# Kernel optimization log

Hardware: AMD Instinct MI355X
Metric: run time of the kernel (lower is better)

The kernel has to match this reference:

```python
import jax, jax.numpy as jnp
import numpy as np

B = 256          # batch of molecules
N_ATOM = 1024    # atoms per molecule
N_EDGE = 8192    # directed edges per molecule (avg degree 8)
NEG_SLOPE = 0.01 # torch LeakyReLU default


def setup_inputs() -> dict:
    key = jax.random.key(0)
    ks = jax.random.split(key, 8)
    x = jax.random.normal(ks[0], (B, 3 * N_ATOM), dtype=jnp.float32)
    edge_index = jax.random.randint(ks[1], (2, N_EDGE), 0, N_ATOM, dtype=jnp.int64)
    # GCNConv weights (Glorot-ish small scale) and biases
    W1 = jax.random.normal(ks[2], (3, 64), dtype=jnp.float32) * 0.3
    b1 = jnp.zeros((64,), jnp.float32)
    W2 = jax.random.normal(ks[3], (64, 64), dtype=jnp.float32) * 0.1
    b2 = jnp.zeros((64,), jnp.float32)
    # project MLP: Linear(64,128) + LeakyReLU
    Wp = jax.random.normal(ks[4], (64, 128), dtype=jnp.float32) * 0.1
    bp = jnp.zeros((128,), jnp.float32)
    return {"x": x, "edge_index": edge_index, "W1": W1, "b1": b1,
            "W2": W2, "b2": b2, "Wp": Wp, "bp": bp}


def _leaky_relu(v):
    return jnp.where(v >= 0, v, NEG_SLOPE * v)


def reference(x, edge_index, W1, b1, W2, b2, Wp, bp):
    # x: [B, 3*n_atom] -> node features [B, n_atom, 3]
    bsz, n_feat = x.shape
    n = n_feat // 3
    h = x.reshape(bsz, n, 3)

    src = edge_index[0]  # message sources
    dst = edge_index[1]  # aggregation targets

    # GCN normalization with self-loops: deg[i] = 1 + in-degree(i)
    ones_e = jnp.ones((src.shape[0],), x.dtype)
    deg = jax.ops.segment_sum(ones_e, dst, num_segments=n) + 1.0
    dinv = jax.lax.rsqrt(deg)                # deg^{-1/2}, deg >= 1
    norm_e = dinv[src] * dinv[dst]           # [E]
    norm_self = dinv * dinv                  # self-loop weight per node

    def gcn(h, W, b):
        hw = h @ W                                        # [B, n, d_out]
        msg = hw[:, src, :] * norm_e[None, :, None]       # [B, E, d_out]
        agg = jax.vmap(lambda m: jax.ops.segment_sum(m, dst, num_segments=n))(msg)
        return agg + norm_self[None, :, None] * hw + b

    h = _leaky_relu(gcn(h, W1, b1))
    h = _leaky_relu(gcn(h, W2, b2))

    # global_mean_pool: every graph has exactly n atoms -> mean over atom axis
    g = h.mean(axis=1)                                    # [B, 64]

    # project MLP: Linear + LeakyReLU
    return _leaky_relu(g @ Wp + bp)                       # [B, 128]
```

## Files before the change

kernel.cpp:

```cpp
#include <hip/hip_runtime.h>

#define N_ATOMS 1024
#define N_EDGES 8192
#define EPAD    (N_EDGES + N_ATOMS)
#define NBATCH  256
#define NEG     0.01f

typedef unsigned int u32;
typedef __attribute__((ext_vector_type(2))) float f32x2;
typedef __attribute__((ext_vector_type(4))) float f32x4;
typedef __attribute__((ext_vector_type(8))) _Float16 f16x8;

__device__ __forceinline__ u32 pkrtz(float lo, float hi) {
    u32 r;
    asm("v_cvt_pkrtz_f16_f32 %0, %1, %2" : "=v"(r) : "v"(lo), "v"(hi));
    return r;
}
#define FMIX_LO(a, w, u) \
    asm("v_fma_mix_f32 %0, %1, %2, %0 op_sel_hi:[0,1,0]" : "+v"(a) : "v"(w), "v"(u))
#define FMIX_HI(a, w, u) \
    asm("v_fma_mix_f32 %0, %1, %2, %0 op_sel:[0,1,0] op_sel_hi:[0,1,0]" : "+v"(a) : "v"(w), "v"(u))

#define ROWPTR_OFF 0
#define COLW_OFF   4352
#define SELFW_OFF  (4352 + 73728)
#define PERM_OFF   (SELFW_OFF + 4096)
#define W2T_OFF    (PERM_OFF + 4096)

#define TSTR_B 144
#define SM_TILE_BYTES (N_ATOMS * TSTR_B)
#define SM_CT_OFF SM_TILE_BYTES
#define SM_TOTAL (SM_TILE_BYTES + 16384)

__global__ __launch_bounds__(1024) void build_csr(
    const int* __restrict__ ei,
    int*  __restrict__ rowptr,
    int2* __restrict__ colw,
    float* __restrict__ selfw_g,
    int*  __restrict__ perm_g,
    u32*  __restrict__ w2t,
    const float* __restrict__ W2)
{
    __shared__ int   sdeg[N_ATOMS];
    __shared__ int   sstart[N_ATOMS];
    __shared__ float sdinv[N_ATOMS];
    __shared__ int   wtot[16];
    __shared__ int   hist[128];
    const int t = threadIdx.x;
    const int lane = t & 63;
    const int w = t >> 6;
    const int* srcA = ei;
    const int* dstA = ei + N_EDGES;

    sdeg[t] = 0;
    if (t < 128) hist[t] = 0;
    for (int e = t; e < EPAD; e += 1024) colw[e] = make_int2(0, 0);
    __syncthreads();
    for (int e = t; e < N_EDGES; e += 1024) atomicAdd(&sdeg[dstA[e]], 1);
    __syncthreads();

    const int deg  = sdeg[t];
    const int pdeg = (deg + 1) & ~1;
    int v = pdeg;
    #pragma unroll
    for (int d = 1; d < 64; d <<= 1) {
        int u = __shfl_up(v, d, 64);
        if (lane >= d) v += u;
    }
    if (lane == 63) wtot[w] = v;
    __syncthreads();
    if (t == 0) {
        int run = 0;
        #pragma unroll
        for (int i = 0; i < 16; ++i) { int c = wtot[i]; wtot[i] = run; run += c; }
    }
    __syncthreads();
    const int start = v - pdeg + wtot[w];
    sstart[t] = start;
    const float dv = rsqrtf((float)deg + 1.0f);
    sdinv[t] = dv;
    rowptr[t] = start;
    if (t == N_ATOMS - 1) rowptr[N_ATOMS] = start + pdeg;
    selfw_g[t] = dv * dv;

    #pragma unroll
    for (int i = 0; i < 2; ++i) {
        const int idx = t + i * 1024;
        const int c = idx >> 5, kk = idx & 31;
        w2t[c * 32 + kk] = pkrtz(W2[(2 * kk) * 64 + c], W2[(2 * kk + 1) * 64 + c]);
    }

    const int dcl = deg < 127 ? deg : 127;
    atomicAdd(&hist[dcl], 1);
    sdeg[t] = 0;
    __syncthreads();
    if (t == 0) {
        int run = 0;
        for (int i = 0; i < 128; ++i) { int c = hist[i]; hist[i] = run; run += c; }
    }
    __syncthreads();
    const int pos = atomicAdd(&hist[dcl], 1);
    perm_g[pos] = t;
    __syncthreads();

    for (int e = t; e < N_EDGES; e += 1024) {
        const int d = dstA[e];
        const int s = srcA[e];
        const int slot = atomicAdd(&sdeg[d], 1);
        const float wgt = sdinv[s] * sdinv[d];
        colw[sstart[d] + slot] = make_int2(s, __float_as_int(wgt));
    }
}

__global__ __launch_bounds__(1024, 4) void gnn_main(
    const float* __restrict__ x,
    const int*  __restrict__ rowptr,
    const int2* __restrict__ colw,
    const float* __restrict__ selfw_g,
    const int*  __restrict__ perm_g,
    const float* __restrict__ W1, const float* __restrict__ b1,
    const u32*  __restrict__ w2t, const float* __restrict__ b2,
    const float* __restrict__ Wp, const float* __restrict__ bp,
    float* __restrict__ out)
{
    extern __shared__ char smem[];
    float4* ctile4 = (float4*)(smem + SM_CT_OFF);
    float*  paux   = (float*)ctile4;
    float*  wpool  = paux;
    float*  gvec   = paux + 1024;
    float*  proj   = paux + 1088;
    int*    satom  = (int*)(paux + 1600);

    const int t = threadIdx.x;
    const int b = blockIdx.x;
    const float* xb = x + (size_t)b * (3 * N_ATOMS);

    {
        float4 c;
        c.x = xb[3 * t]; c.y = xb[3 * t + 1]; c.z = xb[3 * t + 2]; c.w = 0.0f;
        ctile4[t] = c;
    }
    __syncthreads();

    {
        const int atom = perm_g[t];
        const int s0 = rowptr[atom], s1 = rowptr[atom + 1];
        const float sw = selfw_g[atom];
        const float4 cs = ctile4[atom];
        float A0 = sw * cs.x, A1 = sw * cs.y, A2 = sw * cs.z;
        int4 cur = make_int4(0, 0, 0, 0);
        if (s0 < s1) cur = *(const int4*)(colw + s0);
        for (int j = s0; j < s1; j += 2) {
            const int jn = (j + 2 < s1) ? (j + 2) : s0;
            const int4 nxt = *(const int4*)(colw + jn);
            const float4 c0 = ctile4[cur.x];
            const float4 c1 = ctile4[cur.z];
            const float w0 = __int_as_float(cur.y), w1 = __int_as_float(cur.w);
            A0 += w0 * c0.x + w1 * c1.x;
            A1 += w0 * c0.y + w1 * c1.y;
            A2 += w0 * c0.z + w1 * c1.z;
            cur = nxt;
        }
        u32 pw[32];
        #pragma unroll
        for (int p = 0; p < 32; ++p) {
            f32x2 vv = *(const f32x2*)(b1 + 2 * p);
            vv = __builtin_elementwise_fma((f32x2){A0, A0}, *(const f32x2*)(W1 + 2 * p), vv);
            vv = __builtin_elementwise_fma((f32x2){A1, A1}, *(const f32x2*)(W1 + 64 + 2 * p), vv);
            vv = __builtin_elementwise_fma((f32x2){A2, A2}, *(const f32x2*)(W1 + 128 + 2 * p), vv);
            vv.x = fmaxf(vv.x, NEG * vv.x);
            vv.y = fmaxf(vv.y, NEG * vv.y);
            pw[p] = pkrtz(vv.x, vv.y);
        }
        uint4* trow = (uint4*)(smem + (size_t)atom * TSTR_B);
        #pragma unroll
        for (int q = 0; q < 8; ++q)
            trow[q] = make_uint4(pw[4 * q], pw[4 * q + 1], pw[4 * q + 2], pw[4 * q + 3]);
    }
    __syncthreads();

    const int w   = t >> 6;
    const int g   = (t & 63) >> 3;
    const int m   = t & 7;
    const int mo  = m * 16;

    int atoms[8];
    #pragma unroll
    for (int k = 0; k < 8; ++k) atoms[k] = perm_g[k * 128 + w * 8 + g];
    int s0a[8], s1a[8];
    #pragma unroll
    for (int k = 0; k < 8; ++k) {
        s0a[k] = rowptr[atoms[k]];
        s1a[k] = rowptr[atoms[k] + 1];
    }

    u32 pr[8][4];
    #pragma unroll
    for (int k = 0; k < 8; ++k) {
        const int atom = atoms[k];
        float acc[8];
        #pragma unroll
        for (int f = 0; f < 8; ++f) acc[f] = 0.0f;
        {
            const float swk = selfw_g[atom];
            const uint4 sv = *(const uint4*)(smem + (size_t)atom * TSTR_B + mo);
            FMIX_LO(acc[0], swk, sv.x); FMIX_HI(acc[1], swk, sv.x);
            FMIX_LO(acc[2], swk, sv.y); FMIX_HI(acc[3], swk, sv.y);
            FMIX_LO(acc[4], swk, sv.z); FMIX_HI(acc[5], swk, sv.z);
            FMIX_LO(acc[6], swk, sv.w); FMIX_HI(acc[7], swk, sv.w);
        }
        for (int j = s0a[k]; j < s1a[k]; j += 2) {
            const int4 cw = *(const int4*)(colw + j);
            const uint4 qA = *(const uint4*)(smem + (size_t)cw.x * TSTR_B + mo);
            const uint4 qB = *(const uint4*)(smem + (size_t)cw.z * TSTR_B + mo);
            const float wA = __int_as_float(cw.y);
            const float wB = __int_as_float(cw.w);
            FMIX_LO(acc[0], wA, qA.x); FMIX_HI(acc[1], wA, qA.x);
            FMIX_LO(acc[2], wA, qA.y); FMIX_HI(acc[3], wA, qA.y);
            FMIX_LO(acc[4], wA, qA.z); FMIX_HI(acc[5], wA, qA.z);
            FMIX_LO(acc[6], wA, qA.w); FMIX_HI(acc[7], wA, qA.w);
            FMIX_LO(acc[0], wB, qB.x); FMIX_HI(acc[1], wB, qB.x);
            FMIX_LO(acc[2], wB, qB.y); FMIX_HI(acc[3], wB, qB.y);
            FMIX_LO(acc[4], wB, qB.z); FMIX_HI(acc[5], wB, qB.z);
            FMIX_LO(acc[6], wB, qB.w); FMIX_HI(acc[7], wB, qB.w);
        }
        pr[k][0] = pkrtz(acc[0], acc[1]);
        pr[k][1] = pkrtz(acc[2], acc[3]);
        pr[k][2] = pkrtz(acc[4], acc[5]);
        pr[k][3] = pkrtz(acc[6], acc[7]);
    }
    __syncthreads();

    #pragma unroll
    for (int k = 0; k < 8; ++k) {
        *(uint4*)(smem + (size_t)atoms[k] * TSTR_B + mo) =
            make_uint4(pr[k][0], pr[k][1], pr[k][2], pr[k][3]);
    }
    if (m == 0) {
        #pragma unroll
        for (int k = 0; k < 8; ++k) satom[w * 64 + k * 8 + g] = atoms[k];
    }
    __syncthreads();

    {
        const int l15 = t & 15;
        const int lq  = (t & 63) >> 4;

        f16x8 wf[2][4];
        #pragma unroll
        for (int kt = 0; kt < 2; ++kt)
            #pragma unroll
            for (int ct = 0; ct < 4; ++ct)
                wf[kt][ct] = *(const f16x8*)(w2t + (ct * 16 + l15) * 32 + kt * 16 + lq * 4);
        float bias[4];
        #pragma unroll
        for (int ct = 0; ct < 4; ++ct) bias[ct] = b2[ct * 16 + l15];

        float pool[4] = {0.f, 0.f, 0.f, 0.f};
        #pragma unroll
        for (int rt = 0; rt < 4; ++rt) {
            const int arow = satom[w * 64 + rt * 16 + l15];
            const char* ab = smem + (size_t)arow * TSTR_B + lq * 16;
            const f16x8 a0 = *(const f16x8*)(ab);
            const f16x8 a1 = *(const f16x8*)(ab + 64);
            #pragma unroll
            for (int ct = 0; ct < 4; ++ct) {
                f32x4 cf = {0.f, 0.f, 0.f, 0.f};
                cf = __builtin_amdgcn_mfma_f32_16x16x32_f16(a0, wf[0][ct], cf, 0, 0, 0);
                cf = __builtin_amdgcn_mfma_f32_16x16x32_f16(a1, wf[1][ct], cf, 0, 0, 0);
                float s = 0.0f;
                #pragma unroll
                for (int r = 0; r < 4; ++r) {
                    const float vv = cf[r] + bias[ct];
                    s += fmaxf(vv, NEG * vv);
                }
                pool[ct] += s;
            }
        }
        #pragma unroll
        for (int ct = 0; ct < 4; ++ct) {
            pool[ct] += __shfl_xor(pool[ct], 16, 64);
            pool[ct] += __shfl_xor(pool[ct], 32, 64);
        }
        if ((t & 63) < 16) {
            #pragma unroll
            for (int ct = 0; ct < 4; ++ct)
                wpool[w * 64 + ct * 16 + l15] = pool[ct];
        }
    }
    __syncthreads();

    if (t < 64) {
        float s = 0.0f;
        #pragma unroll
        for (int ww = 0; ww < 16; ++ww) s += wpool[ww * 64 + t];
        gvec[t] = s * (1.0f / 1024.0f);
    }
    __syncthreads();
    if (t < 512) {
        const int col = t & 127, pc = t >> 7;
        float s = 0.0f;
        #pragma unroll
        for (int f = 0; f < 16; ++f)
            s += gvec[pc * 16 + f] * Wp[(pc * 16 + f) * 128 + col];
        proj[pc * 128 + col] = s;
    }
    __syncthreads();
    if (t < 128) {
        float s = bp[t] + proj[t] + proj[128 + t] + proj[256 + t] + proj[384 + t];
        s = fmaxf(s, NEG * s);
        out[(size_t)b * 128 + t] = s;
    }
}

extern "C" void kernel_launch(void* const* d_in, const int* in_sizes, int n_in,
                              void* d_out, int out_size, void* d_ws, size_t ws_size,
                              hipStream_t stream) {
    const float* x  = (const float*)d_in[0];
    const int*   ei = (const int*)  d_in[1];
    const float* W1 = (const float*)d_in[2];
    const float* b1 = (const float*)d_in[3];
    const float* W2 = (const float*)d_in[4];
    const float* b2 = (const float*)d_in[5];
    const float* Wp = (const float*)d_in[6];
    const float* bp = (const float*)d_in[7];
    float* out = (float*)d_out;

    char* ws = (char*)d_ws;
    int*   rowptr = (int*)  (ws + ROWPTR_OFF);
    int2*  colw   = (int2*) (ws + COLW_OFF);
    float* selfw  = (float*)(ws + SELFW_OFF);
    int*   perm   = (int*)  (ws + PERM_OFF);
    u32*   w2t    = (u32*)  (ws + W2T_OFF);

    build_csr<<<1, 1024, 0, stream>>>(ei, rowptr, colw, selfw, perm, w2t, W2);

    (void)hipFuncSetAttribute((const void*)gnn_main,
                              hipFuncAttributeMaxDynamicSharedMemorySize, SM_TOTAL);
    gnn_main<<<NBATCH, 1024, SM_TOTAL, stream>>>(
        x, rowptr, colw, selfw, perm, W1, b1, w2t, b2, Wp, bp, out);
}
```

Before: 41.93 us.

## Interleave four atoms per aggregation pass and hoist index/weight loads above barriers

The layer-2 gather loop now processes four atoms together with 32 accumulators, so independent LDS gathers from different atoms can be in flight at once instead of running one atom's edge loop serially. Per-atom rowptr, self-weight and perm loads, and the MFMA weight and bias fragments, are moved ahead of the barriers so their global latency overlaps earlier work. The full zeroing of the padded edge array in the setup kernel is replaced by writing only the single pad slot of odd-degree rows. The cost is higher register pressure and some divergence, since atoms in a group have different degrees.

```diff
diff --git a/kernel.cpp b/kernel.cpp
--- a/kernel.cpp
+++ b/kernel.cpp
@@ -54,7 +54,6 @@
 
     sdeg[t] = 0;
     if (t < 128) hist[t] = 0;
-    for (int e = t; e < EPAD; e += 1024) colw[e] = make_int2(0, 0);
     __syncthreads();
     for (int e = t; e < N_EDGES; e += 1024) atomicAdd(&sdeg[dstA[e]], 1);
     __syncthreads();
@@ -82,6 +81,7 @@
     rowptr[t] = start;
     if (t == N_ATOMS - 1) rowptr[N_ATOMS] = start + pdeg;
     selfw_g[t] = dv * dv;
+    if (deg & 1) colw[start + deg] = make_int2(0, 0);
 
     #pragma unroll
     for (int i = 0; i < 2; ++i) {
@@ -177,58 +177,82 @@
         for (int q = 0; q < 8; ++q)
             trow[q] = make_uint4(pw[4 * q], pw[4 * q + 1], pw[4 * q + 2], pw[4 * q + 3]);
     }
-    __syncthreads();
 
     const int w   = t >> 6;
     const int g   = (t & 63) >> 3;
     const int m   = t & 7;
     const int mo  = m * 16;
 
-    int atoms[8];
-    #pragma unroll
-    for (int k = 0; k < 8; ++k) atoms[k] = perm_g[k * 128 + w * 8 + g];
-    int s0a[8], s1a[8];
+    int atoms[8], s0a[8], npa[8];
+    float swa[8];
     #pragma unroll
     for (int k = 0; k < 8; ++k) {
-        s0a[k] = rowptr[atoms[k]];
-        s1a[k] = rowptr[atoms[k] + 1];
-    }
+        atoms[k] = perm_g[k * 128 + w * 8 + g];
+        const int r0 = rowptr[atoms[k]];
+        const int r1 = rowptr[atoms[k] + 1];
+        s0a[k] = r0;
+        npa[k] = (r1 - r0) >> 1;
+        swa[k] = selfw_g[atoms[k]];
+    }
+    __syncthreads();
 
     u32 pr[8][4];
     #pragma unroll
-    for (int k = 0; k < 8; ++k) {
-        const int atom = atoms[k];
-        float acc[8];
-        #pragma unroll
-        for (int f = 0; f < 8; ++f) acc[f] = 0.0f;
-        {
-            const float swk = selfw_g[atom];
-            const uint4 sv = *(const uint4*)(smem + (size_t)atom * TSTR_B + mo);
-            FMIX_LO(acc[0], swk, sv.x); FMIX_HI(acc[1], swk, sv.x);
-            FMIX_LO(acc[2], swk, sv.y); FMIX_HI(acc[3], swk, sv.y);
-            FMIX_LO(acc[4], swk, sv.z); FMIX_HI(acc[5], swk, sv.z);
-            FMIX_LO(acc[6], swk, sv.w); FMIX_HI(acc[7], swk, sv.w);
-        }
-        for (int j = s0a[k]; j < s1a[k]; j += 2) {
-            const int4 cw = *(const int4*)(colw + j);
-            const uint4 qA = *(const uint4*)(smem + (size_t)cw.x * TSTR_B + mo);
-            const uint4 qB = *(const uint4*)(smem + (size_t)cw.z * TSTR_B + mo);
-            const float wA = __int_as_float(cw.y);
-            const float wB = __int_as_float(cw.w);
-            FMIX_LO(acc[0], wA, qA.x); FMIX_HI(acc[1], wA, qA.x);
-            FMIX_LO(acc[2], wA, qA.y); FMIX_HI(acc[3], wA, qA.y);
-            FMIX_LO(acc[4], wA, qA.z); FMIX_HI(acc[5], wA, qA.z);
-            FMIX_LO(acc[6], wA, qA.w); FMIX_HI(acc[7], wA, qA.w);
-            FMIX_LO(acc[0], wB, qB.x); FMIX_HI(acc[1], wB, qB.x);
-            FMIX_LO(acc[2], wB, qB.y); FMIX_HI(acc[3], wB, qB.y);
-            FMIX_LO(acc[4], wB, qB.z); FMIX_HI(acc[5], wB, qB.z);
-            FMIX_LO(acc[6], wB, qB.w); FMIX_HI(acc[7], wB, qB.w);
-        }
-        pr[k][0] = pkrtz(acc[0], acc[1]);
-        pr[k][1] = pkrtz(acc[2], acc[3]);
-        pr[k][2] = pkrtz(acc[4], acc[5]);
-        pr[k][3] = pkrtz(acc[6], acc[7]);
-    }
+    for (int p = 0; p < 2; ++p) {
+        float acc[32];
+        #pragma unroll
+        for (int f = 0; f < 32; ++f) acc[f] = 0.0f;
+        #pragma unroll
+        for (int k = 0; k < 4; ++k) {
+            const uint4 sv = *(const uint4*)(smem + (size_t)atoms[p*4+k] * TSTR_B + mo);
+            const float swk = swa[p*4+k];
+            FMIX_LO(acc[k*8+0], swk, sv.x); FMIX_HI(acc[k*8+1], swk, sv.x);
+            FMIX_LO(acc[k*8+2], swk, sv.y); FMIX_HI(acc[k*8+3], swk, sv.y);
+            FMIX_LO(acc[k*8+4], swk, sv.z); FMIX_HI(acc[k*8+5], swk, sv.z);
+            FMIX_LO(acc[k*8+6], swk, sv.w); FMIX_HI(acc[k*8+7], swk, sv.w);
+        }
+        const int mx = max(max(npa[p*4+0], npa[p*4+1]), max(npa[p*4+2], npa[p*4+3]));
+        for (int jj = 0; jj < mx; ++jj) {
+            #pragma unroll
+            for (int k = 0; k < 4; ++k) {
+                if (jj < npa[p*4+k]) {
+                    const int4 cw = *(const int4*)(colw + s0a[p*4+k] + 2*jj);
+                    const uint4 qA = *(const uint4*)(smem + (size_t)cw.x * TSTR_B + mo);
+                    const uint4 qB = *(const uint4*)(smem + (size_t)cw.z * TSTR_B + mo);
+                    const float wA = __int_as_float(cw.y);
+                    const float wB = __int_as_float(cw.w);
+                    FMIX_LO(acc[k*8+0], wA, qA.x); FMIX_HI(acc[k*8+1], wA, qA.x);
+                    FMIX_LO(acc[k*8+2], wA, qA.y); FMIX_HI(acc[k*8+3], wA, qA.y);
+                    FMIX_LO(acc[k*8+4], wA, qA.z); FMIX_HI(acc[k*8+5], wA, qA.z);
+                    FMIX_LO(acc[k*8+6], wA, qA.w); FMIX_HI(acc[k*8+7], wA, qA.w);
+                    FMIX_LO(acc[k*8+0], wB, qB.x); FMIX_HI(acc[k*8+1], wB, qB.x);
+                    FMIX_LO(acc[k*8+2], wB, qB.y); FMIX_HI(acc[k*8+3], wB, qB.y);
+                    FMIX_LO(acc[k*8+4], wB, qB.z); FMIX_HI(acc[k*8+5], wB, qB.z);
+                    FMIX_LO(acc[k*8+6], wB, qB.w); FMIX_HI(acc[k*8+7], wB, qB.w);
+                }
+            }
+        }
+        #pragma unroll
+        for (int k = 0; k < 4; ++k) {
+            pr[p*4+k][0] = pkrtz(acc[k*8+0], acc[k*8+1]);
+            pr[p*4+k][1] = pkrtz(acc[k*8+2], acc[k*8+3]);
+            pr[p*4+k][2] = pkrtz(acc[k*8+4], acc[k*8+5]);
+            pr[p*4+k][3] = pkrtz(acc[k*8+6], acc[k*8+7]);
+        }
+    }
+
+    const int l15 = t & 15;
+    const int lq  = (t & 63) >> 4;
+    f16x8 wf[2][4];
+    #pragma unroll
+    for (int kt = 0; kt < 2; ++kt)
+        #pragma unroll
+        for (int ct = 0; ct < 4; ++ct)
+            wf[kt][ct] = *(const f16x8*)(w2t + (ct * 16 + l15) * 32 + kt * 16 + lq * 4);
+    float bias[4];
+    #pragma unroll
+    for (int ct = 0; ct < 4; ++ct) bias[ct] = b2[ct * 16 + l15];
+
     __syncthreads();
 
     #pragma unroll
@@ -243,19 +267,6 @@
     __syncthreads();
 
     {
-        const int l15 = t & 15;
-        const int lq  = (t & 63) >> 4;
-
-        f16x8 wf[2][4];
-        #pragma unroll
-        for (int kt = 0; kt < 2; ++kt)
-            #pragma unroll
-            for (int ct = 0; ct < 4; ++ct)
-                wf[kt][ct] = *(const f16x8*)(w2t + (ct * 16 + l15) * 32 + kt * 16 + lq * 4);
-        float bias[4];
-        #pragma unroll
-        for (int ct = 0; ct < 4; ++ct) bias[ct] = b2[ct * 16 + l15];
-
         float pool[4] = {0.f, 0.f, 0.f, 0.f};
         #pragma unroll
         for (int rt = 0; rt < 4; ++rt) {
```

Result: no change. 41.68 us (-0.6%).

## Store atoms in degree-sorted slot order to drop permutation indirection

Applied to the files above, without the earlier changes.

Relabels atoms by their degree-sorted slot in build_csr: edge sources are rewritten to slot indices, and per-slot metadata (row start, pair count, self weight) is packed. In gnn_main the coordinates are scattered into slot order once, so both GCN layers and the MFMA stage index the tile directly by slot and no longer need perm/rowptr lookups or the satom table. The change also zeroes only the odd padding entry instead of clearing the whole edge array. It hoists metadata, W2 fragment, bias and Wp loads ahead of barriers, and removes one barrier so the layer-1 result write overlaps the metadata loads. In exchange it adds a scattered shared store on input and more live registers.

```diff
diff --git a/kernel.cpp b/kernel.cpp
--- a/kernel.cpp
+++ b/kernel.cpp
@@ -21,11 +21,11 @@
 #define FMIX_HI(a, w, u) \
     asm("v_fma_mix_f32 %0, %1, %2, %0 op_sel:[0,1,0] op_sel_hi:[0,1,0]" : "+v"(a) : "v"(w), "v"(u))
 
-#define ROWPTR_OFF 0
-#define COLW_OFF   4352
-#define SELFW_OFF  (4352 + 73728)
-#define PERM_OFF   (SELFW_OFF + 4096)
-#define W2T_OFF    (PERM_OFF + 4096)
+#define META_OFF   0
+#define COLW_OFF   8192
+#define SELFW_OFF  (8192 + 73728)
+#define IPERM_OFF  (SELFW_OFF + 4096)
+#define W2T_OFF    (IPERM_OFF + 4096)
 
 #define TSTR_B 144
 #define SM_TILE_BYTES (N_ATOMS * TSTR_B)
@@ -34,15 +34,16 @@
 
 __global__ __launch_bounds__(1024) void build_csr(
     const int* __restrict__ ei,
-    int*  __restrict__ rowptr,
     int2* __restrict__ colw,
-    float* __restrict__ selfw_g,
-    int*  __restrict__ perm_g,
+    int2* __restrict__ meta,
+    float* __restrict__ selfw_s,
+    int*  __restrict__ iperm_g,
     u32*  __restrict__ w2t,
     const float* __restrict__ W2)
 {
     __shared__ int   sdeg[N_ATOMS];
     __shared__ int   sstart[N_ATOMS];
+    __shared__ int   siperm[N_ATOMS];
     __shared__ float sdinv[N_ATOMS];
     __shared__ int   wtot[16];
     __shared__ int   hist[128];
@@ -54,7 +55,6 @@
 
     sdeg[t] = 0;
     if (t < 128) hist[t] = 0;
-    for (int e = t; e < EPAD; e += 1024) colw[e] = make_int2(0, 0);
     __syncthreads();
     for (int e = t; e < N_EDGES; e += 1024) atomicAdd(&sdeg[dstA[e]], 1);
     __syncthreads();
@@ -79,9 +79,7 @@
     sstart[t] = start;
     const float dv = rsqrtf((float)deg + 1.0f);
     sdinv[t] = dv;
-    rowptr[t] = start;
-    if (t == N_ATOMS - 1) rowptr[N_ATOMS] = start + pdeg;
-    selfw_g[t] = dv * dv;
+    if (deg & 1) colw[start + deg] = make_int2(0, 0);
 
     #pragma unroll
     for (int i = 0; i < 2; ++i) {
@@ -92,7 +90,6 @@
 
     const int dcl = deg < 127 ? deg : 127;
     atomicAdd(&hist[dcl], 1);
-    sdeg[t] = 0;
     __syncthreads();
     if (t == 0) {
         int run = 0;
@@ -100,7 +97,11 @@
     }
     __syncthreads();
     const int pos = atomicAdd(&hist[dcl], 1);
-    perm_g[pos] = t;
+    siperm[t] = pos;
+    iperm_g[t] = pos;
+    meta[pos] = make_int2(start, pdeg >> 1);
+    selfw_s[pos] = dv * dv;
+    sdeg[t] = 0;
     __syncthreads();
 
     for (int e = t; e < N_EDGES; e += 1024) {
@@ -108,16 +109,16 @@
         const int s = srcA[e];
         const int slot = atomicAdd(&sdeg[d], 1);
         const float wgt = sdinv[s] * sdinv[d];
-        colw[sstart[d] + slot] = make_int2(s, __float_as_int(wgt));
+        colw[sstart[d] + slot] = make_int2(siperm[s], __float_as_int(wgt));
     }
 }
 
 __global__ __launch_bounds__(1024, 4) void gnn_main(
     const float* __restrict__ x,
-    const int*  __restrict__ rowptr,
+    const int2* __restrict__ meta,
     const int2* __restrict__ colw,
-    const float* __restrict__ selfw_g,
-    const int*  __restrict__ perm_g,
+    const float* __restrict__ selfw_s,
+    const int*  __restrict__ iperm_g,
     const float* __restrict__ W1, const float* __restrict__ b1,
     const u32*  __restrict__ w2t, const float* __restrict__ b2,
     const float* __restrict__ Wp, const float* __restrict__ bp,
@@ -129,30 +130,29 @@
     float*  wpool  = paux;
     float*  gvec   = paux + 1024;
     float*  proj   = paux + 1088;
-    int*    satom  = (int*)(paux + 1600);
 
     const int t = threadIdx.x;
     const int b = blockIdx.x;
     const float* xb = x + (size_t)b * (3 * N_ATOMS);
 
     {
+        const int ip = iperm_g[t];
         float4 c;
         c.x = xb[3 * t]; c.y = xb[3 * t + 1]; c.z = xb[3 * t + 2]; c.w = 0.0f;
-        ctile4[t] = c;
+        ctile4[ip] = c;
     }
     __syncthreads();
 
     {
-        const int atom = perm_g[t];
-        const int s0 = rowptr[atom], s1 = rowptr[atom + 1];
-        const float sw = selfw_g[atom];
-        const float4 cs = ctile4[atom];
+        const int2 mt = meta[t];
+        const int s0 = mt.x, np1 = mt.y;
+        const float sw = selfw_s[t];
+        const float4 cs = ctile4[t];
         float A0 = sw * cs.x, A1 = sw * cs.y, A2 = sw * cs.z;
         int4 cur = make_int4(0, 0, 0, 0);
-        if (s0 < s1) cur = *(const int4*)(colw + s0);
-        for (int j = s0; j < s1; j += 2) {
-            const int jn = (j + 2 < s1) ? (j + 2) : s0;
-            const int4 nxt = *(const int4*)(colw + jn);
+        if (np1 > 0) cur = *(const int4*)(colw + s0);
+        for (int jj = 0; jj < np1; ++jj) {
+            const int4 nxt = (jj + 1 < np1) ? *(const int4*)(colw + s0 + 2 * (jj + 1)) : cur;
             const float4 c0 = ctile4[cur.x];
             const float4 c1 = ctile4[cur.z];
             const float w0 = __int_as_float(cur.y), w1 = __int_as_float(cur.w);
@@ -172,44 +172,45 @@
             vv.y = fmaxf(vv.y, NEG * vv.y);
             pw[p] = pkrtz(vv.x, vv.y);
         }
-        uint4* trow = (uint4*)(smem + (size_t)atom * TSTR_B);
+        uint4* trow = (uint4*)(smem + (size_t)t * TSTR_B);
         #pragma unroll
         for (int q = 0; q < 8; ++q)
             trow[q] = make_uint4(pw[4 * q], pw[4 * q + 1], pw[4 * q + 2], pw[4 * q + 3]);
     }
-    __syncthreads();
 
     const int w   = t >> 6;
     const int g   = (t & 63) >> 3;
     const int m   = t & 7;
     const int mo  = m * 16;
 
-    int atoms[8];
-    #pragma unroll
-    for (int k = 0; k < 8; ++k) atoms[k] = perm_g[k * 128 + w * 8 + g];
-    int s0a[8], s1a[8];
+    int s0a[8], npa[8];
+    float swa[8];
     #pragma unroll
     for (int k = 0; k < 8; ++k) {
-        s0a[k] = rowptr[atoms[k]];
-        s1a[k] = rowptr[atoms[k] + 1];
-    }
+        const int slot = k * 128 + w * 8 + g;
+        const int2 mk = meta[slot];
+        s0a[k] = mk.x;
+        npa[k] = mk.y;
+        swa[k] = selfw_s[slot];
+    }
+    __syncthreads();
 
     u32 pr[8][4];
     #pragma unroll
     for (int k = 0; k < 8; ++k) {
-        const int atom = atoms[k];
+        const int slot = k * 128 + w * 8 + g;
         float acc[8];
         #pragma unroll
         for (int f = 0; f < 8; ++f) acc[f] = 0.0f;
         {
-            const float swk = selfw_g[atom];
-            const uint4 sv = *(const uint4*)(smem + (size_t)atom * TSTR_B + mo);
+            const float swk = swa[k];
+            const uint4 sv = *(const uint4*)(smem + (size_t)slot * TSTR_B + mo);
             FMIX_LO(acc[0], swk, sv.x); FMIX_HI(acc[1], swk, sv.x);
             FMIX_LO(acc[2], swk, sv.y); FMIX_HI(acc[3], swk, sv.y);
             FMIX_LO(acc[4], swk, sv.z); FMIX_HI(acc[5], swk, sv.z);
             FMIX_LO(acc[6], swk, sv.w); FMIX_HI(acc[7], swk, sv.w);
         }
-        for (int j = s0a[k]; j < s1a[k]; j += 2) {
+        for (int j = s0a[k]; j < s0a[k] + 2 * npa[k]; j += 2) {
             const int4 cw = *(const int4*)(colw + j);
             const uint4 qA = *(const uint4*)(smem + (size_t)cw.x * TSTR_B + mo);
             const uint4 qB = *(const uint4*)(smem + (size_t)cw.z * TSTR_B + mo);
@@ -229,38 +230,42 @@
         pr[k][2] = pkrtz(acc[4], acc[5]);
         pr[k][3] = pkrtz(acc[6], acc[7]);
     }
+
+    const int l15 = t & 15;
+    const int lq  = (t & 63) >> 4;
+    f16x8 wf[2][4];
+    #pragma unroll
+    for (int kt = 0; kt < 2; ++kt)
+        #pragma unroll
+        for (int ct = 0; ct < 4; ++ct)
+            wf[kt][ct] = *(const f16x8*)(w2t + (ct * 16 + l15) * 32 + kt * 16 + lq * 4);
+    float bias[4];
+    #pragma unroll
+    for (int ct = 0; ct < 4; ++ct) bias[ct] = b2[ct * 16 + l15];
+    float wpv[16];
+    {
+        const int col = t & 127, pc = (t >> 7) & 3;
+        #pragma unroll
+        for (int f = 0; f < 16; ++f)
+            wpv[f] = Wp[(pc * 16 + f) * 128 + col];
+    }
+
     __syncthreads();
 
     #pragma unroll
     for (int k = 0; k < 8; ++k) {
-        *(uint4*)(smem + (size_t)atoms[k] * TSTR_B + mo) =
+        const int slot = k * 128 + w * 8 + g;
+        *(uint4*)(smem + (size_t)slot * TSTR_B + mo) =
             make_uint4(pr[k][0], pr[k][1], pr[k][2], pr[k][3]);
     }
-    if (m == 0) {
-        #pragma unroll
-        for (int k = 0; k < 8; ++k) satom[w * 64 + k * 8 + g] = atoms[k];
-    }
     __syncthreads();
 
     {
-        const int l15 = t & 15;
-        const int lq  = (t & 63) >> 4;
-
-        f16x8 wf[2][4];
-        #pragma unroll
-        for (int kt = 0; kt < 2; ++kt)
-            #pragma unroll
-            for (int ct = 0; ct < 4; ++ct)
-                wf[kt][ct] = *(const f16x8*)(w2t + (ct * 16 + l15) * 32 + kt * 16 + lq * 4);
-        float bias[4];
-        #pragma unroll
-        for (int ct = 0; ct < 4; ++ct) bias[ct] = b2[ct * 16 + l15];
-
         float pool[4] = {0.f, 0.f, 0.f, 0.f};
         #pragma unroll
         for (int rt = 0; rt < 4; ++rt) {
-            const int arow = satom[w * 64 + rt * 16 + l15];
-            const char* ab = smem + (size_t)arow * TSTR_B + lq * 16;
+            const int row = w * 64 + rt * 16 + l15;
+            const char* ab = smem + (size_t)row * TSTR_B + lq * 16;
             const f16x8 a0 = *(const f16x8*)(ab);
             const f16x8 a1 = *(const f16x8*)(ab + 64);
             #pragma unroll
@@ -302,7 +307,7 @@
         float s = 0.0f;
         #pragma unroll
         for (int f = 0; f < 16; ++f)
-            s += gvec[pc * 16 + f] * Wp[(pc * 16 + f) * 128 + col];
+            s += gvec[pc * 16 + f] * wpv[f];
         proj[pc * 128 + col] = s;
     }
     __syncthreads();
@@ -327,16 +332,16 @@
     float* out = (float*)d_out;
 
     char* ws = (char*)d_ws;
-    int*   rowptr = (int*)  (ws + ROWPTR_OFF);
+    int2*  meta   = (int2*) (ws + META_OFF);
     int2*  colw   = (int2*) (ws + COLW_OFF);
     float* selfw  = (float*)(ws + SELFW_OFF);
-    int*   perm   = (int*)  (ws + PERM_OFF);
+    int*   iperm  = (int*)  (ws + IPERM_OFF);
     u32*   w2t    = (u32*)  (ws + W2T_OFF);
 
-    build_csr<<<1, 1024, 0, stream>>>(ei, rowptr, colw, selfw, perm, w2t, W2);
+    build_csr<<<1, 1024, 0, stream>>>(ei, colw, meta, selfw, iperm, w2t, W2);
 
     (void)hipFuncSetAttribute((const void*)gnn_main,
                               hipFuncAttributeMaxDynamicSharedMemorySize, SM_TOTAL);
     gnn_main<<<NBATCH, 1024, SM_TOTAL, stream>>>(
-        x, rowptr, colw, selfw, perm, W1, b1, w2t, b2, Wp, bp, out);
+        x, meta, colw, selfw, iperm, W1, b1, w2t, b2, Wp, bp, out);
 }
```

Result: slower. 43.13 us (+2.9%).
